# Kernel optimization log

Hardware: AMD Instinct MI355X
Metric: run time of the kernel (lower is better)

The kernel has to match this reference:

```python
import jax, jax.numpy as jnp
import numpy as np

B, S, D = 8, 1024, 256


def _linear_params(key, d):
    k1, k2 = jax.random.split(key)
    lim = 1.0 / np.sqrt(d)
    W = jax.random.uniform(k1, (d, d), jnp.float32, -lim, lim)
    b = jax.random.uniform(k2, (d,), jnp.float32, -lim, lim)
    return W, b


def setup_inputs() -> dict:
    key = jax.random.key(0)
    ks = jax.random.split(key, 7)
    x = jax.random.normal(ks[0], (B, S, D), jnp.float32)
    Wq, bq = _linear_params(ks[1], D)
    Wk, bk = _linear_params(ks[2], D)
    Wv, bv = _linear_params(ks[3], D)
    Wf, bf = _linear_params(ks[4], D)
    Wi, bi = _linear_params(ks[5], D)
    Wo, bo = _linear_params(ks[6], D)
    return {"x": x, "Wq": Wq, "bq": bq, "Wk": Wk, "bk": bk, "Wv": Wv, "bv": bv,
            "Wf": Wf, "bf": bf, "Wi": Wi, "bi": bi, "Wo": Wo, "bo": bo}


def reference(x, Wq, bq, Wk, bk, Wv, bv, Wf, bf, Wi, bi, Wo, bo):
    # Projections (torch Linear stores W as [out, in])
    q = x @ Wq.T + bq
    k = x @ Wk.T + bk
    v = x @ Wq.T + bq  # faithful to source: forward uses self.W_q(x) for v (W_v unused)
    f = jax.nn.sigmoid(x @ Wf.T + bf)  # forget gate, sigmoid
    i = jnp.exp(x @ Wi.T + bi)         # input gate, exp

    # time-major xs: each (S, B, D)
    xs = tuple(jnp.swapaxes(a, 0, 1) for a in (f, i, k, v, q))
    C0 = jnp.zeros((x.shape[0], x.shape[2], x.shape[2]), x.dtype)  # matrix memory [B,D,D]
    n0 = jnp.zeros((x.shape[0], x.shape[2]), x.dtype)              # normalizer [B,D]

    def step(carry, t):
        C, n = carry
        ft, it, kt, vt, qt = t
        # C_t = f_t * C_{t-1} + i_t * v_t k_t^T  (gates broadcast over key dim)
        C = ft[:, :, None] * C + it[:, :, None] * (vt[:, :, None] * kt[:, None, :])
        n = ft * n + it * kt
        num = jnp.einsum('bik,bk->bi', C, qt)
        den = jnp.maximum(jnp.abs(jnp.einsum('bk,bk->b', n, qt)), 1.0)[:, None]
        return (C, n), num / den

    _, h = jax.lax.scan(step, (C0, n0), xs)
    h = jnp.swapaxes(h, 0, 1)  # (B, S, D)
    return h @ Wo.T + bo
```

## Files before the change

kernel.cpp:

```cpp
#include <hip/hip_runtime.h>
#include <math.h>

namespace {

constexpr int Bn = 8;
constexpr int Sn = 1024;
constexpr int Dn = 256;
constexpr int Mn = Bn * Sn;
constexpr int L  = 32;
constexpr int NSEG = Sn / L;

typedef __attribute__((ext_vector_type(8))) short short8;
typedef __attribute__((ext_vector_type(4))) float f32x4;

__device__ float g_den[Bn * Sn];

__device__ __forceinline__ float sigmoidf_(float x) {
    return 1.0f / (1.0f + __expf(-x));
}

__device__ __forceinline__ unsigned short f2bf(float x) {
    unsigned int u = __float_as_uint(x);
    return (unsigned short)((u + 0x7FFF + ((u >> 16) & 1)) >> 16);
}
__device__ __forceinline__ float bf2f(unsigned short h) {
    return __uint_as_float(((unsigned int)h) << 16);
}

__global__ __launch_bounds__(256) void proj_gemm(
    const float* __restrict__ X,
    const float* __restrict__ W0, const float* __restrict__ b0,
    const float* __restrict__ W1, const float* __restrict__ b1,
    const float* __restrict__ W2, const float* __restrict__ b2,
    const float* __restrict__ W3, const float* __restrict__ b3,
    float* __restrict__ Y0, float* __restrict__ Y1,
    float* __restrict__ Y2, float* __restrict__ Y3)
{
    __shared__ unsigned short Ah[128][40];
    __shared__ unsigned short Al[128][40];
    __shared__ unsigned short Bh[128][40];
    __shared__ unsigned short Bl[128][40];

    const int tid = threadIdx.x;
    const int mb  = blockIdx.x * 128;
    const int nbg = blockIdx.y;
    const int widx = nbg >> 1;
    const int ro   = (nbg & 1) * 128;

    const float* Wsel = (widx == 0) ? W0 : (widx == 1) ? W1 : (widx == 2) ? W2 : W3;
    const float* bsel = (widx == 0) ? b0 : (widx == 1) ? b1 : (widx == 2) ? b2 : b3;
    float*       Ysel = (widx == 0) ? Y0 : (widx == 1) ? Y1 : (widx == 2) ? Y2 : Y3;

    const int lane = tid & 63;
    const int wv   = tid >> 6;
    const int wm   = (wv >> 1) * 64;
    const int wn   = (wv & 1) * 64;
    const int quad = lane >> 4;
    const int l16  = lane & 15;
    const int srow = tid >> 1;
    const int skq  = (tid & 1) * 16;

    f32x4 acc[4][4];
    #pragma unroll
    for (int mt = 0; mt < 4; ++mt)
        #pragma unroll
        for (int nt = 0; nt < 4; ++nt)
            acc[mt][nt] = (f32x4){0.f, 0.f, 0.f, 0.f};

    for (int k0 = 0; k0 < Dn; k0 += 32) {
        float4 xa[4], wb[4];
        #pragma unroll
        for (int c = 0; c < 4; ++c) {
            xa[c] = *(const float4*)(X    + (size_t)(mb + srow) * Dn + k0 + skq + 4 * c);
            wb[c] = *(const float4*)(Wsel + (size_t)(ro + srow) * Dn + k0 + skq + 4 * c);
        }
        __syncthreads();
        #pragma unroll
        for (int c = 0; c < 4; ++c) {
            const float xs[4] = {xa[c].x, xa[c].y, xa[c].z, xa[c].w};
            const float wsv[4] = {wb[c].x, wb[c].y, wb[c].z, wb[c].w};
            ushort4 h, l;
            unsigned short t0;
            t0 = f2bf(xs[0]); h.x = t0; l.x = f2bf(xs[0] - bf2f(t0));
            t0 = f2bf(xs[1]); h.y = t0; l.y = f2bf(xs[1] - bf2f(t0));
            t0 = f2bf(xs[2]); h.z = t0; l.z = f2bf(xs[2] - bf2f(t0));
            t0 = f2bf(xs[3]); h.w = t0; l.w = f2bf(xs[3] - bf2f(t0));
            *(ushort4*)&Ah[srow][skq + 4 * c] = h;
            *(ushort4*)&Al[srow][skq + 4 * c] = l;
            t0 = f2bf(wsv[0]); h.x = t0; l.x = f2bf(wsv[0] - bf2f(t0));
            t0 = f2bf(wsv[1]); h.y = t0; l.y = f2bf(wsv[1] - bf2f(t0));
            t0 = f2bf(wsv[2]); h.z = t0; l.z = f2bf(wsv[2] - bf2f(t0));
            t0 = f2bf(wsv[3]); h.w = t0; l.w = f2bf(wsv[3] - bf2f(t0));
            *(ushort4*)&Bh[srow][skq + 4 * c] = h;
            *(ushort4*)&Bl[srow][skq + 4 * c] = l;
        }
        __syncthreads();

        short8 afh[4], afl[4];
        #pragma unroll
        for (int mt = 0; mt < 4; ++mt) {
            const int row = wm + mt * 16 + l16;
            afh[mt] = *(const short8*)&Ah[row][quad * 8];
            afl[mt] = *(const short8*)&Al[row][quad * 8];
        }
        #pragma unroll
        for (int nt = 0; nt < 4; ++nt) {
            const int row = wn + nt * 16 + l16;
            const short8 bfh = *(const short8*)&Bh[row][quad * 8];
            const short8 bfl = *(const short8*)&Bl[row][quad * 8];
            #pragma unroll
            for (int mt = 0; mt < 4; ++mt) {
                acc[mt][nt] = __builtin_amdgcn_mfma_f32_16x16x32_bf16(
                    afh[mt], bfh, acc[mt][nt], 0, 0, 0);
                acc[mt][nt] = __builtin_amdgcn_mfma_f32_16x16x32_bf16(
                    afh[mt], bfl, acc[mt][nt], 0, 0, 0);
                acc[mt][nt] = __builtin_amdgcn_mfma_f32_16x16x32_bf16(
                    afl[mt], bfh, acc[mt][nt], 0, 0, 0);
            }
        }
    }

    #pragma unroll
    for (int nt = 0; nt < 4; ++nt) {
        const int col = ro + wn + nt * 16 + l16;
        const float bv = bsel[col];
        #pragma unroll
        for (int mt = 0; mt < 4; ++mt) {
            const int rowb = mb + wm + mt * 16 + quad * 4;
            #pragma unroll
            for (int r = 0; r < 4; ++r) {
                float v = acc[mt][nt][r] + bv;
                if (widx == 2)      v = sigmoidf_(v);
                else if (widx == 3) v = __expf(v);
                Ysel[(size_t)(rowb + r) * Dn + col] = v;
            }
        }
    }
}

__global__ __launch_bounds__(256) void out_gemm(
    const float* __restrict__ X, const float* __restrict__ W,
    const float* __restrict__ bias, float* __restrict__ Y)
{
    __shared__ unsigned short Ah[128][40];
    __shared__ unsigned short Al[128][40];
    __shared__ unsigned short Bh[128][40];
    __shared__ unsigned short Bl[128][40];

    const int tid = threadIdx.x;
    const int mb  = blockIdx.x * 128;
    const int nb  = blockIdx.y * 128;

    const int lane = tid & 63;
    const int wv   = tid >> 6;
    const int wm   = (wv >> 1) * 64;
    const int wn   = (wv & 1) * 64;
    const int quad = lane >> 4;
    const int l16  = lane & 15;
    const int srow = tid >> 1;
    const int skq  = (tid & 1) * 16;

    const float invd = 1.0f / fmaxf(fabsf(g_den[mb + srow]), 1.0f);

    f32x4 acc[4][4];
    #pragma unroll
    for (int mt = 0; mt < 4; ++mt)
        #pragma unroll
        for (int nt = 0; nt < 4; ++nt)
            acc[mt][nt] = (f32x4){0.f, 0.f, 0.f, 0.f};

    for (int k0 = 0; k0 < Dn; k0 += 32) {
        float4 xa[4], wb[4];
        #pragma unroll
        for (int c = 0; c < 4; ++c) {
            xa[c] = *(const float4*)(X + (size_t)(mb + srow) * Dn + k0 + skq + 4 * c);
            wb[c] = *(const float4*)(W + (size_t)(nb + srow) * Dn + k0 + skq + 4 * c);
            xa[c].x *= invd; xa[c].y *= invd; xa[c].z *= invd; xa[c].w *= invd;
        }
        __syncthreads();
        #pragma unroll
        for (int c = 0; c < 4; ++c) {
            const float xs[4] = {xa[c].x, xa[c].y, xa[c].z, xa[c].w};
            const float wsv[4] = {wb[c].x, wb[c].y, wb[c].z, wb[c].w};
            ushort4 h, l;
            unsigned short t0;
            t0 = f2bf(xs[0]); h.x = t0; l.x = f2bf(xs[0] - bf2f(t0));
            t0 = f2bf(xs[1]); h.y = t0; l.y = f2bf(xs[1] - bf2f(t0));
            t0 = f2bf(xs[2]); h.z = t0; l.z = f2bf(xs[2] - bf2f(t0));
            t0 = f2bf(xs[3]); h.w = t0; l.w = f2bf(xs[3] - bf2f(t0));
            *(ushort4*)&Ah[srow][skq + 4 * c] = h;
            *(ushort4*)&Al[srow][skq + 4 * c] = l;
            t0 = f2bf(wsv[0]); h.x = t0; l.x = f2bf(wsv[0] - bf2f(t0));
            t0 = f2bf(wsv[1]); h.y = t0; l.y = f2bf(wsv[1] - bf2f(t0));
            t0 = f2bf(wsv[2]); h.z = t0; l.z = f2bf(wsv[2] - bf2f(t0));
            t0 = f2bf(wsv[3]); h.w = t0; l.w = f2bf(wsv[3] - bf2f(t0));
            *(ushort4*)&Bh[srow][skq + 4 * c] = h;
            *(ushort4*)&Bl[srow][skq + 4 * c] = l;
        }
        __syncthreads();

        short8 afh[4], afl[4];
        #pragma unroll
        for (int mt = 0; mt < 4; ++mt) {
            const int row = wm + mt * 16 + l16;
            afh[mt] = *(const short8*)&Ah[row][quad * 8];
            afl[mt] = *(const short8*)&Al[row][quad * 8];
        }
        #pragma unroll
        for (int nt = 0; nt < 4; ++nt) {
            const int row = wn + nt * 16 + l16;
            const short8 bfh = *(const short8*)&Bh[row][quad * 8];
            const short8 bfl = *(const short8*)&Bl[row][quad * 8];
            #pragma unroll
            for (int mt = 0; mt < 4; ++mt) {
                acc[mt][nt] = __builtin_amdgcn_mfma_f32_16x16x32_bf16(
                    afh[mt], bfh, acc[mt][nt], 0, 0, 0);
                acc[mt][nt] = __builtin_amdgcn_mfma_f32_16x16x32_bf16(
                    afh[mt], bfl, acc[mt][nt], 0, 0, 0);
                acc[mt][nt] = __builtin_amdgcn_mfma_f32_16x16x32_bf16(
                    afl[mt], bfh, acc[mt][nt], 0, 0, 0);
            }
        }
    }

    #pragma unroll
    for (int nt = 0; nt < 4; ++nt) {
        const int col = nb + wn + nt * 16 + l16;
        const float bv = bias[col];
        #pragma unroll
        for (int mt = 0; mt < 4; ++mt) {
            const int rowb = mb + wm + mt * 16 + quad * 4;
            #pragma unroll
            for (int r = 0; r < 4; ++r) {
                Y[(size_t)(rowb + r) * Dn + col] = acc[mt][nt][r] + bv;
            }
        }
    }
}

__global__ __launch_bounds__(256) void prep(
    const float* __restrict__ Pf, const float* __restrict__ Pi,
    const float* __restrict__ Pk, const float* __restrict__ Pq,
    float* __restrict__ Gc, float* __restrict__ Vt, float* __restrict__ Nt,
    float* __restrict__ Aend, float* __restrict__ un, float* __restrict__ Ssm)
{
    const int m = blockIdx.x;
    const int b = blockIdx.y;
    const int tid = threadIdx.x;

    if (tid < L) g_den[b * Sn + m * L + tid] = 0.0f;

    {
        const int r = tid;
        const size_t base = (size_t)b * Sn * Dn + (size_t)m * L * Dn + r;
        float G = 1.0f, Nacc = 0.0f;
        #pragma unroll 4
        for (int t = 0; t < L; ++t) {
            const size_t off = base + (size_t)t * Dn;
            const float f  = Pf[off];
            const float iv = Pi[off];
            const float kv = Pk[off];
            const float vv = Pq[off];
            G *= f;
            const float rG = 1.0f / G;
            Gc[off] = G;
            Vt[off] = iv * vv * rG;
            Nacc = fmaf(iv * kv, rG, Nacc);
            Nt[off] = Nacc;
        }
        const size_t s = ((size_t)b * NSEG + m) * Dn + r;
        Aend[s] = G;
        un[s]   = G * Nacc;
    }

    {
        const size_t qb = (size_t)b * Sn * Dn + (size_t)m * L * Dn;
        const int tau = tid >> 3;
        const int s4  = (tid & 7) * 4;

        float a0 = 0.f, a1 = 0.f, a2 = 0.f, a3 = 0.f;
        #pragma unroll 4
        for (int c = 0; c < Dn; c += 4) {
            const float4 q4 = *(const float4*)(Pq + qb + (size_t)tau * Dn + c);
            const float4 k0 = *(const float4*)(Pk + qb + (size_t)(s4 + 0) * Dn + c);
            const float4 k1 = *(const float4*)(Pk + qb + (size_t)(s4 + 1) * Dn + c);
            const float4 k2 = *(const float4*)(Pk + qb + (size_t)(s4 + 2) * Dn + c);
            const float4 k3 = *(const float4*)(Pk + qb + (size_t)(s4 + 3) * Dn + c);
            a0 += q4.x*k0.x + q4.y*k0.y + q4.z*k0.z + q4.w*k0.w;
            a1 += q4.x*k1.x + q4.y*k1.y + q4.z*k1.z + q4.w*k1.w;
            a2 += q4.x*k2.x + q4.y*k2.y + q4.z*k2.z + q4.w*k2.w;
            a3 += q4.x*k3.x + q4.y*k3.y + q4.z*k3.z + q4.w*k3.w;
        }
        float* outp = Ssm + ((size_t)b * NSEG + m) * L * L + (size_t)tau * L + s4;
        outp[0] = (s4 + 0 <= tau) ? a0 : 0.0f;
        outp[1] = (s4 + 1 <= tau) ? a1 : 0.0f;
        outp[2] = (s4 + 2 <= tau) ? a2 : 0.0f;
        outp[3] = (s4 + 3 <= tau) ? a3 : 0.0f;
    }
}

__global__ __launch_bounds__(256) void ut_gemm(
    const float* __restrict__ Pk, const float* __restrict__ Vt,
    const float* __restrict__ Aend, float* __restrict__ UT)
{
    __shared__ float As[L][68];
    __shared__ float Bs[L][68];

    const int bm   = blockIdx.x;
    const int tile = blockIdx.y;
    const int cb   = (tile >> 2) * 64;
    const int rb   = (tile & 3) * 64;
    const int b    = bm >> 5;
    const int m    = bm & 31;
    const size_t kb = (size_t)b * Sn * Dn + (size_t)m * L * Dn;
    const int tid = threadIdx.x;

    #pragma unroll
    for (int n = 0; n < 8; ++n) {
        const int e  = n * 256 + tid;
        const int sg = e >> 6;
        const int cc = e & 63;
        As[sg][cc] = Pk[kb + (size_t)sg * Dn + cb + cc];
        Bs[sg][cc] = Vt[kb + (size_t)sg * Dn + rb + cc];
    }
    __syncthreads();

    const int tx = tid & 15;
    const int ty = tid >> 4;
    float acc[4][4];
    #pragma unroll
    for (int i = 0; i < 4; ++i)
        #pragma unroll
        for (int j = 0; j < 4; ++j) acc[i][j] = 0.0f;

    #pragma unroll
    for (int sg = 0; sg < L; ++sg) {
        const float4 a4 = *(const float4*)&As[sg][ty * 4];
        const float4 b4 = *(const float4*)&Bs[sg][tx * 4];
        const float aa[4] = {a4.x, a4.y, a4.z, a4.w};
        const float bb[4] = {b4.x, b4.y, b4.z, b4.w};
        #pragma unroll
        for (int i = 0; i < 4; ++i)
            #pragma unroll
            for (int j = 0; j < 4; ++j)
                acc[i][j] = fmaf(aa[i], bb[j], acc[i][j]);
    }

    const float4 g4 = *(const float4*)(Aend + (size_t)bm * Dn + rb + tx * 4);
    float* ub = UT + (size_t)bm * Dn * Dn;
    #pragma unroll
    for (int i = 0; i < 4; ++i) {
        float4 o;
        o.x = acc[i][0] * g4.x; o.y = acc[i][1] * g4.y;
        o.z = acc[i][2] * g4.z; o.w = acc[i][3] * g4.w;
        *(float4*)(ub + (size_t)(cb + ty * 4 + i) * Dn + rb + tx * 4) = o;
    }
}

__global__ __launch_bounds__(256) void compose(
    const float* __restrict__ UT, const float* __restrict__ Aend,
    const float* __restrict__ un,
    float* __restrict__ CinT, float* __restrict__ nin)
{
    const int gx = blockIdx.x;
    const int b  = blockIdx.y;
    const int tid = threadIdx.x;

    if (gx == 64) {
        const int r = tid;
        float acc = 0.0f;
        for (int m = 0; m < NSEG; ++m) {
            const size_t s = ((size_t)b * NSEG + m) * Dn + r;
            nin[s] = acc;
            acc = fmaf(Aend[s], acc, un[s]);
        }
        return;
    }

    const int id = gx * 256 + tid;
    const int c  = id >> 6;
    const int r4 = (id & 63) * 4;

    float4 acc = make_float4(0.f, 0.f, 0.f, 0.f);
    for (int m = 0; m < NSEG; ++m) {
        const size_t bm  = (size_t)b * NSEG + m;
        const size_t idx = bm * Dn * Dn + (size_t)c * Dn + r4;
        *(float4*)(CinT + idx) = acc;
        const float4 a4 = *(const float4*)(Aend + bm * Dn + r4);
        const float4 u4 = *(const float4*)(UT + idx);
        acc.x = fmaf(a4.x, acc.x, u4.x);
        acc.y = fmaf(a4.y, acc.y, u4.y);
        acc.z = fmaf(a4.z, acc.z, u4.z);
        acc.w = fmaf(a4.w, acc.w, u4.w);
    }
}

__global__ __launch_bounds__(256) void num_gemm(
    const float* __restrict__ Pq, const float* __restrict__ Vt,
    const float* __restrict__ Gc, const float* __restrict__ Ssm,
    const float* __restrict__ CinT, const float* __restrict__ Nt,
    const float* __restrict__ nin, float* __restrict__ Pnum)
{
    __shared__ float Sld[L][33];
    __shared__ float Qld[L][257];

    const int rb = blockIdx.x * 128;
    const int m  = blockIdx.y;
    const int b  = blockIdx.z;
    const size_t qb = (size_t)b * Sn * Dn + (size_t)m * L * Dn;
    const size_t ub = ((size_t)b * NSEG + m) * Dn * Dn;
    const size_t sb = ((size_t)b * NSEG + m) * L * L;
    const int tid = threadIdx.x;

    #pragma unroll
    for (int n = 0; n < 4; ++n) {
        const int e = n * 256 + tid;
        Sld[e >> 5][e & 31] = Ssm[sb + e];
    }
    #pragma unroll
    for (int n = 0; n < L; ++n)
        Qld[n][tid] = Pq[qb + (size_t)n * Dn + tid];
    __syncthreads();

    const int tx = tid & 31;
    const int ty = tid >> 5;
    const int r4 = rb + tx * 4;
    const int t4 = ty * 4;

    float4 acc[4];
    #pragma unroll
    for (int i = 0; i < 4; ++i) acc[i] = make_float4(0.f, 0.f, 0.f, 0.f);

    #pragma unroll 4
    for (int sg = 0; sg < L; ++sg) {
        const float4 v4 = *(const float4*)(Vt + qb + (size_t)sg * Dn + r4);
        #pragma unroll
        for (int i = 0; i < 4; ++i) {
            const float s = Sld[t4 + i][sg];
            acc[i].x = fmaf(s, v4.x, acc[i].x);
            acc[i].y = fmaf(s, v4.y, acc[i].y);
            acc[i].z = fmaf(s, v4.z, acc[i].z);
            acc[i].w = fmaf(s, v4.w, acc[i].w);
        }
    }

    #pragma unroll 8
    for (int c = 0; c < Dn; ++c) {
        const float4 ct = *(const float4*)(CinT + ub + (size_t)c * Dn + r4);
        #pragma unroll
        for (int i = 0; i < 4; ++i) {
            const float q = Qld[t4 + i][c];
            acc[i].x = fmaf(q, ct.x, acc[i].x);
            acc[i].y = fmaf(q, ct.y, acc[i].y);
            acc[i].z = fmaf(q, ct.z, acc[i].z);
            acc[i].w = fmaf(q, ct.w, acc[i].w);
        }
    }

    const float4 i4 = *(const float4*)(nin + ((size_t)b * NSEG + m) * Dn + r4);
    float dp[4];
    #pragma unroll
    for (int i = 0; i < 4; ++i) {
        const size_t off = qb + (size_t)(t4 + i) * Dn + r4;
        const float4 g4 = *(const float4*)(Gc + off);
        const float4 q4 = *(const float4*)(Pq + off);
        const float4 n4 = *(const float4*)(Nt + off);
        float4 o;
        o.x = acc[i].x * g4.x; o.y = acc[i].y * g4.y;
        o.z = acc[i].z * g4.z; o.w = acc[i].w * g4.w;
        *(float4*)(Pnum + off) = o;
        dp[i] = q4.x * g4.x * (i4.x + n4.x)
              + q4.y * g4.y * (i4.y + n4.y)
              + q4.z * g4.z * (i4.z + n4.z)
              + q4.w * g4.w * (i4.w + n4.w);
    }

    #pragma unroll
    for (int s = 1; s < 32; s <<= 1) {
        #pragma unroll
        for (int i = 0; i < 4; ++i)
            dp[i] += __shfl_xor(dp[i], s, 64);
    }
    if (tx == 0) {
        #pragma unroll
        for (int i = 0; i < 4; ++i)
            atomicAdd(&g_den[b * Sn + m * L + t4 + i], dp[i]);
    }
}

}

extern "C" void kernel_launch(void* const* d_in, const int* in_sizes, int n_in,
                              void* d_out, int out_size, void* d_ws, size_t ws_size,
                              hipStream_t stream)
{
    const float* x  = (const float*)d_in[0];
    const float* Wq = (const float*)d_in[1];  const float* bq = (const float*)d_in[2];
    const float* Wk = (const float*)d_in[3];  const float* bk = (const float*)d_in[4];
    const float* Wf = (const float*)d_in[7];  const float* bf = (const float*)d_in[8];
    const float* Wi = (const float*)d_in[9];  const float* bi = (const float*)d_in[10];
    const float* Wo = (const float*)d_in[11]; const float* bo = (const float*)d_in[12];
    float* out = (float*)d_out;

    float* ws = (float*)d_ws;
    const size_t sz = (size_t)Mn * Dn;
    float* Pq = ws;
    float* Pk = ws + sz;
    float* Pf = ws + 2 * sz;
    float* Pi = ws + 3 * sz;
    float* Pn = ws + 4 * sz;
    float* Gc = ws + 5 * sz;
    float* Vt = ws + 6 * sz;
    float* Nt = ws + 7 * sz;
    float* UT   = ws + 8 * sz;
    float* CinT = ws + 16 * sz;
    float* Ssm  = ws + 24 * sz;
    float* Aend = Ssm + (size_t)Bn * NSEG * L * L;
    float* un   = Aend + (size_t)Bn * NSEG * Dn;
    float* nin  = un   + (size_t)Bn * NSEG * Dn;

    proj_gemm<<<dim3(Mn / 128, 8), 256, 0, stream>>>(
        x, Wq, bq, Wk, bk, Wf, bf, Wi, bi, Pq, Pk, Pf, Pi);

    prep<<<dim3(NSEG, Bn), 256, 0, stream>>>(
        Pf, Pi, Pk, Pq, Gc, Vt, Nt, Aend, un, Ssm);

    ut_gemm<<<dim3(Bn * NSEG, 16), 256, 0, stream>>>(Pk, Vt, Aend, UT);

    compose<<<dim3(65, Bn), 256, 0, stream>>>(UT, Aend, un, CinT, nin);

    num_gemm<<<dim3(2, NSEG, Bn), 256, 0, stream>>>(
        Pq, Vt, Gc, Ssm, CinT, Nt, nin, Pn);

    out_gemm<<<dim3(Mn / 128, Dn / 128), 256, 0, stream>>>(Pn, Wo, bo, out);
}
```

Measured before the change: 229.8 us.

## Pre-split GEMM operands into bf16 hi/lo buffers and prefetch in GEMMs

Adds separate kernels that convert X, the projection weights, the normalized Pn and Wo into bf16 hi/lo pairs once, stored in reused workspace regions. The projection and output GEMMs then load pre-split bf16 data with register prefetch of the next k-tile instead of converting fp32 tiles in every block. This removes the repeated split work, which each block previously redid for shared operands. The output GEMM also moves to 64x64 tiles for more blocks. The cost is two extra launches and an extra round trip through global memory for the split data.

```diff
diff --git a/kernel.cpp b/kernel.cpp
--- a/kernel.cpp
+++ b/kernel.cpp
@@ -27,19 +27,84 @@
     return __uint_as_float(((unsigned int)h) << 16);
 }
 
-__global__ __launch_bounds__(256) void proj_gemm(
+__global__ __launch_bounds__(256) void split_xw(
     const float* __restrict__ X,
-    const float* __restrict__ W0, const float* __restrict__ b0,
-    const float* __restrict__ W1, const float* __restrict__ b1,
-    const float* __restrict__ W2, const float* __restrict__ b2,
-    const float* __restrict__ W3, const float* __restrict__ b3,
+    const float* __restrict__ Wq, const float* __restrict__ Wk,
+    const float* __restrict__ Wf, const float* __restrict__ Wi,
+    unsigned short* __restrict__ Xh, unsigned short* __restrict__ Xl,
+    unsigned short* __restrict__ Wh, unsigned short* __restrict__ Wl)
+{
+    const int i = blockIdx.x * 256 + threadIdx.x;
+    const float4* src;
+    unsigned short* dh;
+    unsigned short* dl;
+    size_t off;
+    if (i < 524288) {
+        src = (const float4*)X + i;
+        dh = Xh; dl = Xl;
+        off = (size_t)i * 4;
+    } else {
+        const int j = i - 524288;
+        const int w = j >> 14;
+        const int r = j & 16383;
+        const float* Wp = (w == 0) ? Wq : (w == 1) ? Wk : (w == 2) ? Wf : Wi;
+        src = (const float4*)Wp + r;
+        dh = Wh; dl = Wl;
+        off = ((size_t)w << 16) + (size_t)r * 4;
+    }
+    const float4 v = *src;
+    ushort4 h, l;
+    h.x = f2bf(v.x); l.x = f2bf(v.x - bf2f(h.x));
+    h.y = f2bf(v.y); l.y = f2bf(v.y - bf2f(h.y));
+    h.z = f2bf(v.z); l.z = f2bf(v.z - bf2f(h.z));
+    h.w = f2bf(v.w); l.w = f2bf(v.w - bf2f(h.w));
+    *(ushort4*)(dh + off) = h;
+    *(ushort4*)(dl + off) = l;
+}
+
+__global__ __launch_bounds__(256) void split_pn(
+    const float* __restrict__ Pn, const float* __restrict__ Wo,
+    unsigned short* __restrict__ Ph, unsigned short* __restrict__ Pl,
+    unsigned short* __restrict__ Woh, unsigned short* __restrict__ Wol)
+{
+    const int i = blockIdx.x * 256 + threadIdx.x;
+    float4 v;
+    unsigned short* dh;
+    unsigned short* dl;
+    size_t off;
+    if (i < 524288) {
+        const float invd = 1.0f / fmaxf(fabsf(g_den[i >> 6]), 1.0f);
+        v = ((const float4*)Pn)[i];
+        v.x *= invd; v.y *= invd; v.z *= invd; v.w *= invd;
+        dh = Ph; dl = Pl;
+        off = (size_t)i * 4;
+    } else {
+        const int j = i - 524288;
+        v = ((const float4*)Wo)[j];
+        dh = Woh; dl = Wol;
+        off = (size_t)j * 4;
+    }
+    ushort4 h, l;
+    h.x = f2bf(v.x); l.x = f2bf(v.x - bf2f(h.x));
+    h.y = f2bf(v.y); l.y = f2bf(v.y - bf2f(h.y));
+    h.z = f2bf(v.z); l.z = f2bf(v.z - bf2f(h.z));
+    h.w = f2bf(v.w); l.w = f2bf(v.w - bf2f(h.w));
+    *(ushort4*)(dh + off) = h;
+    *(ushort4*)(dl + off) = l;
+}
+
+__global__ __launch_bounds__(256) void proj_gemm2(
+    const unsigned short* __restrict__ Xh, const unsigned short* __restrict__ Xl,
+    const unsigned short* __restrict__ Wh, const unsigned short* __restrict__ Wl,
+    const float* __restrict__ b0, const float* __restrict__ b1,
+    const float* __restrict__ b2, const float* __restrict__ b3,
     float* __restrict__ Y0, float* __restrict__ Y1,
     float* __restrict__ Y2, float* __restrict__ Y3)
 {
-    __shared__ unsigned short Ah[128][40];
-    __shared__ unsigned short Al[128][40];
-    __shared__ unsigned short Bh[128][40];
-    __shared__ unsigned short Bl[128][40];
+    __shared__ unsigned short Ahs[128][40];
+    __shared__ unsigned short Als[128][40];
+    __shared__ unsigned short Bhs[128][40];
+    __shared__ unsigned short Bls[128][40];
 
     const int tid = threadIdx.x;
     const int mb  = blockIdx.x * 128;
@@ -47,7 +112,6 @@
     const int widx = nbg >> 1;
     const int ro   = (nbg & 1) * 128;
 
-    const float* Wsel = (widx == 0) ? W0 : (widx == 1) ? W1 : (widx == 2) ? W2 : W3;
     const float* bsel = (widx == 0) ? b0 : (widx == 1) ? b1 : (widx == 2) ? b2 : b3;
     float*       Ysel = (widx == 0) ? Y0 : (widx == 1) ? Y1 : (widx == 2) ? Y2 : Y3;
 
@@ -60,6 +124,9 @@
     const int srow = tid >> 1;
     const int skq  = (tid & 1) * 16;
 
+    const size_t abase = (size_t)(mb + srow) * Dn + skq;
+    const size_t bbase = (size_t)(nbg * 128 + srow) * Dn + skq;
+
     f32x4 acc[4][4];
     #pragma unroll
     for (int mt = 0; mt < 4; ++mt)
@@ -67,47 +134,45 @@
         for (int nt = 0; nt < 4; ++nt)
             acc[mt][nt] = (f32x4){0.f, 0.f, 0.f, 0.f};
 
+    short8 pah0, pah1, pal0, pal1, pbh0, pbh1, pbl0, pbl1;
+    pah0 = *(const short8*)(Xh + abase);     pah1 = *(const short8*)(Xh + abase + 8);
+    pal0 = *(const short8*)(Xl + abase);     pal1 = *(const short8*)(Xl + abase + 8);
+    pbh0 = *(const short8*)(Wh + bbase);     pbh1 = *(const short8*)(Wh + bbase + 8);
+    pbl0 = *(const short8*)(Wl + bbase);     pbl1 = *(const short8*)(Wl + bbase + 8);
+
     for (int k0 = 0; k0 < Dn; k0 += 32) {
-        float4 xa[4], wb[4];
-        #pragma unroll
-        for (int c = 0; c < 4; ++c) {
-            xa[c] = *(const float4*)(X    + (size_t)(mb + srow) * Dn + k0 + skq + 4 * c);
-            wb[c] = *(const float4*)(Wsel + (size_t)(ro + srow) * Dn + k0 + skq + 4 * c);
-        }
         __syncthreads();
-        #pragma unroll
-        for (int c = 0; c < 4; ++c) {
-            const float xs[4] = {xa[c].x, xa[c].y, xa[c].z, xa[c].w};
-            const float wsv[4] = {wb[c].x, wb[c].y, wb[c].z, wb[c].w};
-            ushort4 h, l;
-            unsigned short t0;
-            t0 = f2bf(xs[0]); h.x = t0; l.x = f2bf(xs[0] - bf2f(t0));
-            t0 = f2bf(xs[1]); h.y = t0; l.y = f2bf(xs[1] - bf2f(t0));
-            t0 = f2bf(xs[2]); h.z = t0; l.z = f2bf(xs[2] - bf2f(t0));
-            t0 = f2bf(xs[3]); h.w = t0; l.w = f2bf(xs[3] - bf2f(t0));
-            *(ushort4*)&Ah[srow][skq + 4 * c] = h;
-            *(ushort4*)&Al[srow][skq + 4 * c] = l;
-            t0 = f2bf(wsv[0]); h.x = t0; l.x = f2bf(wsv[0] - bf2f(t0));
-            t0 = f2bf(wsv[1]); h.y = t0; l.y = f2bf(wsv[1] - bf2f(t0));
-            t0 = f2bf(wsv[2]); h.z = t0; l.z = f2bf(wsv[2] - bf2f(t0));
-            t0 = f2bf(wsv[3]); h.w = t0; l.w = f2bf(wsv[3] - bf2f(t0));
-            *(ushort4*)&Bh[srow][skq + 4 * c] = h;
-            *(ushort4*)&Bl[srow][skq + 4 * c] = l;
-        }
+        *(short8*)&Ahs[srow][skq]     = pah0;
+        *(short8*)&Ahs[srow][skq + 8] = pah1;
+        *(short8*)&Als[srow][skq]     = pal0;
+        *(short8*)&Als[srow][skq + 8] = pal1;
+        *(short8*)&Bhs[srow][skq]     = pbh0;
+        *(short8*)&Bhs[srow][skq + 8] = pbh1;
+        *(short8*)&Bls[srow][skq]     = pbl0;
+        *(short8*)&Bls[srow][skq + 8] = pbl1;
         __syncthreads();
+
+        if (k0 + 32 < Dn) {
+            const size_t ka = abase + k0 + 32;
+            const size_t kb = bbase + k0 + 32;
+            pah0 = *(const short8*)(Xh + ka); pah1 = *(const short8*)(Xh + ka + 8);
+            pal0 = *(const short8*)(Xl + ka); pal1 = *(const short8*)(Xl + ka + 8);
+            pbh0 = *(const short8*)(Wh + kb); pbh1 = *(const short8*)(Wh + kb + 8);
+            pbl0 = *(const short8*)(Wl + kb); pbl1 = *(const short8*)(Wl + kb + 8);
+        }
 
         short8 afh[4], afl[4];
         #pragma unroll
         for (int mt = 0; mt < 4; ++mt) {
             const int row = wm + mt * 16 + l16;
-            afh[mt] = *(const short8*)&Ah[row][quad * 8];
-            afl[mt] = *(const short8*)&Al[row][quad * 8];
+            afh[mt] = *(const short8*)&Ahs[row][quad * 8];
+            afl[mt] = *(const short8*)&Als[row][quad * 8];
         }
         #pragma unroll
         for (int nt = 0; nt < 4; ++nt) {
             const int row = wn + nt * 16 + l16;
-            const short8 bfh = *(const short8*)&Bh[row][quad * 8];
-            const short8 bfl = *(const short8*)&Bl[row][quad * 8];
+            const short8 bfh = *(const short8*)&Bhs[row][quad * 8];
+            const short8 bfl = *(const short8*)&Bls[row][quad * 8];
             #pragma unroll
             for (int mt = 0; mt < 4; ++mt) {
                 acc[mt][nt] = __builtin_amdgcn_mfma_f32_16x16x32_bf16(
@@ -138,81 +203,76 @@
     }
 }
 
-__global__ __launch_bounds__(256) void out_gemm(
-    const float* __restrict__ X, const float* __restrict__ W,
+__global__ __launch_bounds__(256) void out_gemm2(
+    const unsigned short* __restrict__ Ph, const unsigned short* __restrict__ Pl,
+    const unsigned short* __restrict__ Woh, const unsigned short* __restrict__ Wol,
     const float* __restrict__ bias, float* __restrict__ Y)
 {
-    __shared__ unsigned short Ah[128][40];
-    __shared__ unsigned short Al[128][40];
-    __shared__ unsigned short Bh[128][40];
-    __shared__ unsigned short Bl[128][40];
+    __shared__ unsigned short Ahs[64][40];
+    __shared__ unsigned short Als[64][40];
+    __shared__ unsigned short Bhs[64][40];
+    __shared__ unsigned short Bls[64][40];
 
     const int tid = threadIdx.x;
-    const int mb  = blockIdx.x * 128;
-    const int nb  = blockIdx.y * 128;
+    const int mb  = blockIdx.x * 64;
+    const int nb  = blockIdx.y * 64;
 
     const int lane = tid & 63;
     const int wv   = tid >> 6;
-    const int wm   = (wv >> 1) * 64;
-    const int wn   = (wv & 1) * 64;
+    const int wm   = (wv >> 1) * 32;
+    const int wn   = (wv & 1) * 32;
     const int quad = lane >> 4;
     const int l16  = lane & 15;
-    const int srow = tid >> 1;
-    const int skq  = (tid & 1) * 16;
-
-    const float invd = 1.0f / fmaxf(fabsf(g_den[mb + srow]), 1.0f);
-
-    f32x4 acc[4][4];
-    #pragma unroll
-    for (int mt = 0; mt < 4; ++mt)
-        #pragma unroll
-        for (int nt = 0; nt < 4; ++nt)
+    const int srow = tid >> 2;
+    const int skq  = (tid & 3) * 8;
+
+    const size_t abase = (size_t)(mb + srow) * Dn + skq;
+    const size_t bbase = (size_t)(nb + srow) * Dn + skq;
+
+    f32x4 acc[2][2];
+    #pragma unroll
+    for (int mt = 0; mt < 2; ++mt)
+        #pragma unroll
+        for (int nt = 0; nt < 2; ++nt)
             acc[mt][nt] = (f32x4){0.f, 0.f, 0.f, 0.f};
 
+    short8 pah, pal, pbh, pbl;
+    pah = *(const short8*)(Ph  + abase);
+    pal = *(const short8*)(Pl  + abase);
+    pbh = *(const short8*)(Woh + bbase);
+    pbl = *(const short8*)(Wol + bbase);
+
     for (int k0 = 0; k0 < Dn; k0 += 32) {
-        float4 xa[4], wb[4];
-        #pragma unroll
-        for (int c = 0; c < 4; ++c) {
-            xa[c] = *(const float4*)(X + (size_t)(mb + srow) * Dn + k0 + skq + 4 * c);
-            wb[c] = *(const float4*)(W + (size_t)(nb + srow) * Dn + k0 + skq + 4 * c);
-            xa[c].x *= invd; xa[c].y *= invd; xa[c].z *= invd; xa[c].w *= invd;
-        }
         __syncthreads();
-        #pragma unroll
-        for (int c = 0; c < 4; ++c) {
-            const float xs[4] = {xa[c].x, xa[c].y, xa[c].z, xa[c].w};
-            const float wsv[4] = {wb[c].x, wb[c].y, wb[c].z, wb[c].w};
-            ushort4 h, l;
-            unsigned short t0;
-            t0 = f2bf(xs[0]); h.x = t0; l.x = f2bf(xs[0] - bf2f(t0));
-            t0 = f2bf(xs[1]); h.y = t0; l.y = f2bf(xs[1] - bf2f(t0));
-            t0 = f2bf(xs[2]); h.z = t0; l.z = f2bf(xs[2] - bf2f(t0));
-            t0 = f2bf(xs[3]); h.w = t0; l.w = f2bf(xs[3] - bf2f(t0));
-            *(ushort4*)&Ah[srow][skq + 4 * c] = h;
-            *(ushort4*)&Al[srow][skq + 4 * c] = l;
-            t0 = f2bf(wsv[0]); h.x = t0; l.x = f2bf(wsv[0] - bf2f(t0));
-            t0 = f2bf(wsv[1]); h.y = t0; l.y = f2bf(wsv[1] - bf2f(t0));
-            t0 = f2bf(wsv[2]); h.z = t0; l.z = f2bf(wsv[2] - bf2f(t0));
-            t0 = f2bf(wsv[3]); h.w = t0; l.w = f2bf(wsv[3] - bf2f(t0));
-            *(ushort4*)&Bh[srow][skq + 4 * c] = h;
-            *(ushort4*)&Bl[srow][skq + 4 * c] = l;
-        }
+        *(short8*)&Ahs[srow][skq] = pah;
+        *(short8*)&Als[srow][skq] = pal;
+        *(short8*)&Bhs[srow][skq] = pbh;
+        *(short8*)&Bls[srow][skq] = pbl;
         __syncthreads();
 
-        short8 afh[4], afl[4];
-        #pragma unroll
-        for (int mt = 0; mt < 4; ++mt) {
+        if (k0 + 32 < Dn) {
+            const size_t ka = abase + k0 + 32;
+            const size_t kb = bbase + k0 + 32;
+            pah = *(const short8*)(Ph  + ka);
+            pal = *(const short8*)(Pl  + ka);
+            pbh = *(const short8*)(Woh + kb);
+            pbl = *(const short8*)(Wol + kb);
+        }
+
+        short8 afh[2], afl[2];
+        #pragma unroll
+        for (int mt = 0; mt < 2; ++mt) {
             const int row = wm + mt * 16 + l16;
-            afh[mt] = *(const short8*)&Ah[row][quad * 8];
-            afl[mt] = *(const short8*)&Al[row][quad * 8];
-        }
-        #pragma unroll
-        for (int nt = 0; nt < 4; ++nt) {
+            afh[mt] = *(const short8*)&Ahs[row][quad * 8];
+            afl[mt] = *(const short8*)&Als[row][quad * 8];
+        }
+        #pragma unroll
+        for (int nt = 0; nt < 2; ++nt) {
             const int row = wn + nt * 16 + l16;
-            const short8 bfh = *(const short8*)&Bh[row][quad * 8];
-            const short8 bfl = *(const short8*)&Bl[row][quad * 8];
+            const short8 bfh = *(const short8*)&Bhs[row][quad * 8];
+            const short8 bfl = *(const short8*)&Bls[row][quad * 8];
             #pragma unroll
-            for (int mt = 0; mt < 4; ++mt) {
+            for (int mt = 0; mt < 2; ++mt) {
                 acc[mt][nt] = __builtin_amdgcn_mfma_f32_16x16x32_bf16(
                     afh[mt], bfh, acc[mt][nt], 0, 0, 0);
                 acc[mt][nt] = __builtin_amdgcn_mfma_f32_16x16x32_bf16(
@@ -224,11 +284,11 @@
     }
 
     #pragma unroll
-    for (int nt = 0; nt < 4; ++nt) {
+    for (int nt = 0; nt < 2; ++nt) {
         const int col = nb + wn + nt * 16 + l16;
         const float bv = bias[col];
         #pragma unroll
-        for (int mt = 0; mt < 4; ++mt) {
+        for (int mt = 0; mt < 2; ++mt) {
             const int rowb = mb + wm + mt * 16 + quad * 4;
             #pragma unroll
             for (int r = 0; r < 4; ++r) {
@@ -519,8 +579,19 @@
     float* un   = Aend + (size_t)Bn * NSEG * Dn;
     float* nin  = un   + (size_t)Bn * NSEG * Dn;
 
-    proj_gemm<<<dim3(Mn / 128, 8), 256, 0, stream>>>(
-        x, Wq, bq, Wk, bk, Wf, bf, Wi, bi, Pq, Pk, Pf, Pi);
+    unsigned short* Xh = (unsigned short*)UT;
+    unsigned short* Xl = Xh + sz;
+    unsigned short* Wh = Xl + sz;
+    unsigned short* Wl = Wh + (size_t)1024 * Dn;
+    unsigned short* Ph  = (unsigned short*)UT;
+    unsigned short* Pl  = Ph + sz;
+    unsigned short* Woh = (unsigned short*)Ssm;
+    unsigned short* Wol = Woh + (size_t)Dn * Dn;
+
+    split_xw<<<dim3(2304), 256, 0, stream>>>(x, Wq, Wk, Wf, Wi, Xh, Xl, Wh, Wl);
+
+    proj_gemm2<<<dim3(Mn / 128, 8), 256, 0, stream>>>(
+        Xh, Xl, Wh, Wl, bq, bk, bf, bi, Pq, Pk, Pf, Pi);
 
     prep<<<dim3(NSEG, Bn), 256, 0, stream>>>(
         Pf, Pi, Pk, Pq, Gc, Vt, Nt, Aend, un, Ssm);
@@ -532,5 +603,8 @@
     num_gemm<<<dim3(2, NSEG, Bn), 256, 0, stream>>>(
         Pq, Vt, Gc, Ssm, CinT, Nt, nin, Pn);
 
-    out_gemm<<<dim3(Mn / 128, Dn / 128), 256, 0, stream>>>(Pn, Wo, bo, out);
-}
+    split_pn<<<dim3(2112), 256, 0, stream>>>(Pn, Wo, Ph, Pl, Woh, Wol);
+
+    out_gemm2<<<dim3(Mn / 64, Dn / 64), 256, 0, stream>>>(
+        Ph, Pl, Woh, Wol, bo, out);
+}
```

New measurement: 227.7 us. About the same (-0.9%).
